# Kernel tuning notes

Measured on AMD Instinct MI355X. Metric: run time of the kernel, lower is better.

The kernel has to match this reference:

```python
import jax, jax.numpy as jnp
import numpy as np

N = 50000
E = 1600000
F_IN = 128
F_OUT = 64
NEG_SLOPE = 0.2


def setup_inputs() -> dict:
    key = jax.random.key(0)
    k1, k2, k3, k4, k5, k6 = jax.random.split(key, 6)
    x = jax.random.normal(k1, (N, F_IN), dtype=jnp.float32)
    edge_index = jax.random.randint(k2, (2, E), 0, N, dtype=jnp.int64)
    # GATConv params (heads=1): glorot-ish scale
    W = jax.random.normal(k3, (F_IN, F_OUT), dtype=jnp.float32) * (1.0 / np.sqrt(F_IN))
    att_src = jax.random.normal(k4, (F_OUT,), dtype=jnp.float32) * (1.0 / np.sqrt(F_OUT))
    att_dst = jax.random.normal(k5, (F_OUT,), dtype=jnp.float32) * (1.0 / np.sqrt(F_OUT))
    bias = jnp.zeros((F_OUT,), dtype=jnp.float32)
    return {"x": x, "edge_index": edge_index, "W": W, "att_src": att_src, "att_dst": att_dst, "bias": bias}


def _gat_forward(x, edge_index, W, att_src, att_dst, bias):
    n = x.shape[0]
    # add self loops (PyG GATConv default)
    loops = jnp.arange(n, dtype=edge_index.dtype)
    src = jnp.concatenate([edge_index[0], loops])  # [E+N]
    dst = jnp.concatenate([edge_index[1], loops])  # [E+N]

    h = x @ W                                      # [N, F_OUT]
    a_src = h @ att_src                            # [N]
    a_dst = h @ att_dst                            # [N]

    e = a_src[src] + a_dst[dst]                    # [E+N]
    e = jnp.where(e > 0, e, NEG_SLOPE * e)         # LeakyReLU(0.2)

    # softmax over edges grouped by destination node
    e_max = jax.ops.segment_max(e, dst, num_segments=n)     # [N]
    e_exp = jnp.exp(e - e_max[dst])                          # [E+N]
    e_sum = jax.ops.segment_sum(e_exp, dst, num_segments=n)  # [N]
    alpha = e_exp / e_sum[dst]                               # [E+N]

    msg = h[src] * alpha[:, None]                            # [E+N, F_OUT]
    out = jax.ops.segment_sum(msg, dst, num_segments=n)      # [N, F_OUT]
    out = out + bias
    return jax.nn.relu(out)


def reference(x, edge_index, W, att_src, att_dst, bias):
    return _gat_forward(x, edge_index, W, att_src, att_dst, bias)
```

## Files before the change

### kernel.cpp

```cpp
#include <hip/hip_runtime.h>

#define NN 50000
#define NE 1600000
#define FIN 128
#define FOUT 64
#define SLOPE 0.2f

#define NBC  63
#define NPC  800
#define CAPC 27500
#define NBF  1575
#define NPB  32
#define CAPB 1536
#define FBLK 522
#define CHC4 768
#define K2PB 8
#define FINB (NBC * K2PB)
#define GBLK 782
#define LW   136

typedef unsigned int u32;
typedef short short8 __attribute__((ext_vector_type(8)));
typedef float f32x4 __attribute__((ext_vector_type(4)));

__device__ __forceinline__ unsigned short f2bf(float f) {
    u32 u = __float_as_uint(f);
    u += 0x7FFFu + ((u >> 16) & 1u);
    return (unsigned short)(u >> 16);
}
__device__ __forceinline__ float bf2f(unsigned short s) {
    return __uint_as_float(((u32)s) << 16);
}

__global__ __launch_bounds__(256) void fill_k(
        const int* __restrict__ ei, int* __restrict__ ccur,
        u32* __restrict__ cstage) {
    __shared__ int cnt[4][64];
    __shared__ int gb[64];
    __shared__ int cur[64];
    const int tid = threadIdx.x, wv = tid >> 6;
    ((int*)cnt)[tid] = 0;
    __syncthreads();
    const int4* sd4 = (const int4*)(ei + NE);
    const int4* ss4 = (const int4*)ei;
    const int lo = blockIdx.x * CHC4, hi = min(NE / 4, lo + CHC4);
    for (int i = lo + tid; i < hi; i += 256) {
        int4 d = sd4[i];
        atomicAdd(&cnt[wv][d.x / NPC], 1);
        atomicAdd(&cnt[wv][d.y / NPC], 1);
        atomicAdd(&cnt[wv][d.z / NPC], 1);
        atomicAdd(&cnt[wv][d.w / NPC], 1);
    }
    __syncthreads();
    if (tid < NBC) {
        int tot = cnt[0][tid] + cnt[1][tid] + cnt[2][tid] + cnt[3][tid];
        gb[tid] = tot ? atomicAdd(&ccur[tid], tot) : 0;
        cur[tid] = 0;
    }
    __syncthreads();
    for (int i = lo + tid; i < hi; i += 256) {
        int4 d = sd4[i];
        int4 s = ss4[i];
        int b, pos;
        b = d.x / NPC; pos = gb[b] + atomicAdd(&cur[b], 1);
        if (pos < CAPC) cstage[b * CAPC + pos] = (u32)s.x | ((u32)(d.x - b * NPC) << 16);
        b = d.y / NPC; pos = gb[b] + atomicAdd(&cur[b], 1);
        if (pos < CAPC) cstage[b * CAPC + pos] = (u32)s.y | ((u32)(d.y - b * NPC) << 16);
        b = d.z / NPC; pos = gb[b] + atomicAdd(&cur[b], 1);
        if (pos < CAPC) cstage[b * CAPC + pos] = (u32)s.z | ((u32)(d.z - b * NPC) << 16);
        b = d.w / NPC; pos = gb[b] + atomicAdd(&cur[b], 1);
        if (pos < CAPC) cstage[b * CAPC + pos] = (u32)s.w | ((u32)(d.w - b * NPC) << 16);
    }
}

union FgLds {
    unsigned short Wt[64 * LW];
    struct { int cnt[4][32]; int gb[32]; int cur[32]; } f;
};

__global__ __launch_bounds__(256) void fg_k(
        const u32* __restrict__ cstage, const int* __restrict__ ccur,
        int* __restrict__ fcur, u32* __restrict__ fstage,
        const float* __restrict__ x, const float* __restrict__ W,
        const float* __restrict__ att_s, const float* __restrict__ att_d,
        unsigned short* __restrict__ h, float* __restrict__ a_src,
        float* __restrict__ a_dst) {
    __shared__ FgLds L;
    const int tid = threadIdx.x;

    if (blockIdx.x < FINB) {
        const int bin = blockIdx.x / K2PB, sub = blockIdx.x % K2PB;
        const int size = min(ccur[bin], CAPC);
        const int qs = (size + K2PB - 1) / K2PB;
        const int lo = sub * qs, hi = min(size, lo + qs);
        const u32* src = cstage + (size_t)bin * CAPC;
        const int wv = tid >> 6;
        ((int*)L.f.cnt)[tid & 127] = 0;
        __syncthreads();
        for (int i = lo + tid; i < hi; i += 256)
            atomicAdd(&L.f.cnt[wv][(src[i] >> 16) >> 5], 1);
        __syncthreads();
        if (tid < 25) {
            int tot = L.f.cnt[0][tid] + L.f.cnt[1][tid]
                    + L.f.cnt[2][tid] + L.f.cnt[3][tid];
            L.f.gb[tid] = tot ? atomicAdd(&fcur[bin * 25 + tid], tot) : 0;
            L.f.cur[tid] = 0;
        }
        __syncthreads();
        for (int i = lo + tid; i < hi; i += 256) {
            u32 w = src[i];
            int dl = w >> 16;
            int f = dl >> 5;
            int pos = L.f.gb[f] + atomicAdd(&L.f.cur[f], 1);
            if (pos < CAPB)
                fstage[(size_t)(bin * 25 + f) * CAPB + pos] =
                    (w & 0xFFFFu) | ((u32)(dl & 31) << 16);
        }
    } else {
        unsigned short* Wt = L.Wt;
        const int node0 = (blockIdx.x - FINB) * 64;
        for (int i = tid; i < 128 * 16; i += 256) {
            int k = i >> 4, f = (i & 15) * 4;
            float4 w4 = ((const float4*)W)[i];
            Wt[(f + 0) * LW + k] = f2bf(w4.x);
            Wt[(f + 1) * LW + k] = f2bf(w4.y);
            Wt[(f + 2) * LW + k] = f2bf(w4.z);
            Wt[(f + 3) * LW + k] = f2bf(w4.w);
        }
        const int wv = tid >> 6, lane = tid & 63;
        const int q = lane >> 4, mr = lane & 15;
        const int row = node0 + wv * 16 + mr;
        const bool valid = row < NN;
        const float4* x4 = (const float4*)x;

        short8 afr[4];
        #pragma unroll
        for (int ks = 0; ks < 4; ++ks) {
            float4 f0 = make_float4(0.f, 0.f, 0.f, 0.f), f1 = f0;
            if (valid) {
                f0 = x4[(size_t)row * 32 + ks * 8 + q * 2];
                f1 = x4[(size_t)row * 32 + ks * 8 + q * 2 + 1];
            }
            short8 a;
            a[0] = (short)f2bf(f0.x); a[1] = (short)f2bf(f0.y);
            a[2] = (short)f2bf(f0.z); a[3] = (short)f2bf(f0.w);
            a[4] = (short)f2bf(f1.x); a[5] = (short)f2bf(f1.y);
            a[6] = (short)f2bf(f1.z); a[7] = (short)f2bf(f1.w);
            afr[ks] = a;
        }
        __syncthreads();

        f32x4 acc[4] = {{0,0,0,0},{0,0,0,0},{0,0,0,0},{0,0,0,0}};
        #pragma unroll
        for (int ks = 0; ks < 4; ++ks) {
            #pragma unroll
            for (int nt = 0; nt < 4; ++nt) {
                short8 b = *(const short8*)(Wt + (nt * 16 + mr) * LW + ks * 32 + q * 8);
                acc[nt] = __builtin_amdgcn_mfma_f32_16x16x32_bf16(afr[ks], b, acc[nt], 0, 0, 0);
            }
        }
        float atts[4], attd[4];
        #pragma unroll
        for (int nt = 0; nt < 4; ++nt) {
            atts[nt] = att_s[nt * 16 + mr];
            attd[nt] = att_d[nt * 16 + mr];
        }
        #pragma unroll
        for (int r = 0; r < 4; ++r) {
            int node = node0 + wv * 16 + q * 4 + r;
            float ps = 0.f, pd = 0.f;
            #pragma unroll
            for (int nt = 0; nt < 4; ++nt) {
                float v = acc[nt][r];
                if (node < NN) h[(size_t)node * 64 + nt * 16 + mr] = f2bf(v);
                ps += v * atts[nt];
                pd += v * attd[nt];
            }
            #pragma unroll
            for (int off = 8; off > 0; off >>= 1) {
                ps += __shfl_xor(ps, off);
                pd += __shfl_xor(pd, off);
            }
            if (mr == 0 && node < NN) { a_src[node] = ps; a_dst[node] = pd; }
        }
    }
}

__global__ __launch_bounds__(256) void agg_k(
        const u32* __restrict__ staging, const int* __restrict__ bcur,
        const float* __restrict__ a_src, const float* __restrict__ a_dst,
        const ushort4* __restrict__ h4, const float* __restrict__ bias,
        float* __restrict__ out) {
    const int bkt = blockIdx.x;
    const int node0 = bkt << 5;
    if (node0 >= NN) return;
    const int nNodes = min(NPB, NN - node0);
    const int bsize = min(bcur[bkt], CAPB);
    const u32* stg = staging + (size_t)bkt * CAPB;
    const int tid = threadIdx.x, wv = tid >> 6, lane = tid & 63;

    __shared__ u32 pk[CAPB];
    __shared__ unsigned short ssrc[CAPB];
    __shared__ int lcnt[NPB];
    __shared__ int lbase[NPB + 1];
    __shared__ int lcur[NPB];
    float* evals = (float*)pk;

    for (int j = tid; j < bsize; j += 256) pk[j] = stg[j];
    if (tid < NPB) lcnt[tid] = 0;
    __syncthreads();
    for (int j = tid; j < bsize; j += 256)
        atomicAdd(&lcnt[pk[j] >> 16], 1);
    __syncthreads();
    if (tid < 64) {
        int v = (tid < NPB) ? lcnt[tid] : 0;
        #pragma unroll
        for (int off = 1; off < NPB; off <<= 1) {
            int u = __shfl_up(v, off);
            if (tid >= off) v += u;
        }
        if (tid < NPB) lbase[tid + 1] = v;
        if (tid == 0) lbase[0] = 0;
    }
    if (tid >= 64 && tid < 64 + NPB) lcur[tid - 64] = 0;
    __syncthreads();
    for (int j = tid; j < bsize; j += 256) {
        u32 w = pk[j];
        int ld = w >> 16;
        int pos = lbase[ld] + atomicAdd(&lcur[ld], 1);
        ssrc[pos] = (unsigned short)(w & 0xFFFFu);
    }
    __syncthreads();

    const int q = lane >> 4, ql = lane & 15;
    const float4 b4 = ((const float4*)bias)[ql];
    #pragma unroll
    for (int rnd = 0; rnd < 2; ++rnd) {
        const int ln = rnd * 16 + wv * 4 + q;
        if (ln >= nNodes) continue;
        const int n = node0 + ln;
        const int st = lbase[ln], deg = lbase[ln + 1] - st;
        const float ad = a_dst[n];
        float es = a_src[n] + ad; es = es > 0.f ? es : SLOPE * es;
        const float ps = __expf(es);
        float sum = 0.f;
        for (int j = ql; j < deg; j += 16) {
            int s = ssrc[st + j];
            float e = a_src[s] + ad; e = e > 0.f ? e : SLOPE * e;
            float pe = __expf(e);
            evals[st + j] = pe;
            sum += pe;
        }
        sum += __shfl_xor(sum, 8); sum += __shfl_xor(sum, 4);
        sum += __shfl_xor(sum, 2); sum += __shfl_xor(sum, 1);
        const float inv = 1.f / (sum + ps);

        ushort4 hs = h4[(size_t)n * 16 + ql];
        float a0 = ps * bf2f(hs.x), a1 = ps * bf2f(hs.y);
        float a2 = ps * bf2f(hs.z), a3 = ps * bf2f(hs.w);
        int j = 0;
        for (; j + 4 <= deg; j += 4) {
            int s0 = ssrc[st + j], s1 = ssrc[st + j + 1];
            int s2 = ssrc[st + j + 2], s3 = ssrc[st + j + 3];
            float e0 = evals[st + j], e1 = evals[st + j + 1];
            float e2 = evals[st + j + 2], e3 = evals[st + j + 3];
            ushort4 v0 = h4[(size_t)s0 * 16 + ql];
            ushort4 v1 = h4[(size_t)s1 * 16 + ql];
            ushort4 v2 = h4[(size_t)s2 * 16 + ql];
            ushort4 v3 = h4[(size_t)s3 * 16 + ql];
            a0 += e0 * bf2f(v0.x); a1 += e0 * bf2f(v0.y);
            a2 += e0 * bf2f(v0.z); a3 += e0 * bf2f(v0.w);
            a0 += e1 * bf2f(v1.x); a1 += e1 * bf2f(v1.y);
            a2 += e1 * bf2f(v1.z); a3 += e1 * bf2f(v1.w);
            a0 += e2 * bf2f(v2.x); a1 += e2 * bf2f(v2.y);
            a2 += e2 * bf2f(v2.z); a3 += e2 * bf2f(v2.w);
            a0 += e3 * bf2f(v3.x); a1 += e3 * bf2f(v3.y);
            a2 += e3 * bf2f(v3.z); a3 += e3 * bf2f(v3.w);
        }
        for (; j < deg; ++j) {
            int s = ssrc[st + j];
            float ev = evals[st + j];
            ushort4 hv = h4[(size_t)s * 16 + ql];
            a0 += ev * bf2f(hv.x); a1 += ev * bf2f(hv.y);
            a2 += ev * bf2f(hv.z); a3 += ev * bf2f(hv.w);
        }
        float4 o;
        o.x = a0 * inv + b4.x; o.x = o.x > 0.f ? o.x : 0.f;
        o.y = a1 * inv + b4.y; o.y = o.y > 0.f ? o.y : 0.f;
        o.z = a2 * inv + b4.z; o.z = o.z > 0.f ? o.z : 0.f;
        o.w = a3 * inv + b4.w; o.w = o.w > 0.f ? o.w : 0.f;
        ((float4*)out)[(size_t)n * 16 + ql] = o;
    }
}

extern "C" void kernel_launch(void* const* d_in, const int* in_sizes, int n_in,
                              void* d_out, int out_size, void* d_ws, size_t ws_size,
                              hipStream_t stream) {
    const float* x     = (const float*)d_in[0];
    const int*   ei    = (const int*)d_in[1];
    const float* W     = (const float*)d_in[2];
    const float* att_s = (const float*)d_in[3];
    const float* att_d = (const float*)d_in[4];
    const float* bias  = (const float*)d_in[5];
    float* out = (float*)d_out;

    unsigned short* h = (unsigned short*)d_ws;
    float* a_src  = (float*)(h + (size_t)NN * 64);
    float* a_dst  = a_src + NN;
    int*   ccur   = (int*)(a_dst + NN);
    int*   fcur   = ccur + 64;
    u32*   cstage = (u32*)(fcur + 1600);
    u32*   fstage = cstage + (size_t)NBC * CAPC;

    hipMemsetAsync(ccur, 0, (64 + 1600) * sizeof(int), stream);

    fill_k<<<FBLK, 256, 0, stream>>>(ei, ccur, cstage);
    fg_k<<<FINB + GBLK, 256, 0, stream>>>(cstage, ccur, fcur, fstage,
                                          x, W, att_s, att_d, h, a_src, a_dst);
    agg_k<<<NBF, 256, 0, stream>>>(fstage, fcur, a_src, a_dst,
                                   (const ushort4*)h, bias, out);
}
```

Baseline: 146.1 us.

## Use per-wave LDS cursors in binning, double fine-bin split, unroll gather by 8

The coarse and fine binning kernels now turn their per-wave LDS histograms into per-wave prefix offsets after the global atomic. Each wave then claims slots from its own counter instead of one shared block cursor, which cuts LDS atomic contention and drops the separate gb/cur arrays. The fine-binning pass splits each coarse bin across 16 blocks instead of 8 for more parallelism, at the cost of more global atomics on fcur. The aggregation loop unrolls the neighbor gather to 8 so more bf16 row loads are in flight, which raises register use.

```diff
diff --git a/kernel.cpp b/kernel.cpp
--- a/kernel.cpp
+++ b/kernel.cpp
@@ -14,7 +14,7 @@
 #define CAPB 1536
 #define FBLK 522
 #define CHC4 768
-#define K2PB 8
+#define K2PB 16
 #define FINB (NBC * K2PB)
 #define GBLK 782
 #define LW   136
@@ -36,8 +36,6 @@
         const int* __restrict__ ei, int* __restrict__ ccur,
         u32* __restrict__ cstage) {
     __shared__ int cnt[4][64];
-    __shared__ int gb[64];
-    __shared__ int cur[64];
     const int tid = threadIdx.x, wv = tid >> 6;
     ((int*)cnt)[tid] = 0;
     __syncthreads();
@@ -52,30 +50,35 @@
         atomicAdd(&cnt[wv][d.w / NPC], 1);
     }
     __syncthreads();
-    if (tid < NBC) {
-        int tot = cnt[0][tid] + cnt[1][tid] + cnt[2][tid] + cnt[3][tid];
-        gb[tid] = tot ? atomicAdd(&ccur[tid], tot) : 0;
-        cur[tid] = 0;
+    if (tid < 64) {
+        int c0 = cnt[0][tid], c1 = cnt[1][tid];
+        int c2 = cnt[2][tid], c3 = cnt[3][tid];
+        int tot = c0 + c1 + c2 + c3;
+        int base = tot ? atomicAdd(&ccur[tid], tot) : 0;
+        cnt[0][tid] = base;
+        cnt[1][tid] = base + c0;
+        cnt[2][tid] = base + c0 + c1;
+        cnt[3][tid] = base + c0 + c1 + c2;
     }
     __syncthreads();
     for (int i = lo + tid; i < hi; i += 256) {
         int4 d = sd4[i];
         int4 s = ss4[i];
         int b, pos;
-        b = d.x / NPC; pos = gb[b] + atomicAdd(&cur[b], 1);
+        b = d.x / NPC; pos = atomicAdd(&cnt[wv][b], 1);
         if (pos < CAPC) cstage[b * CAPC + pos] = (u32)s.x | ((u32)(d.x - b * NPC) << 16);
-        b = d.y / NPC; pos = gb[b] + atomicAdd(&cur[b], 1);
+        b = d.y / NPC; pos = atomicAdd(&cnt[wv][b], 1);
         if (pos < CAPC) cstage[b * CAPC + pos] = (u32)s.y | ((u32)(d.y - b * NPC) << 16);
-        b = d.z / NPC; pos = gb[b] + atomicAdd(&cur[b], 1);
+        b = d.z / NPC; pos = atomicAdd(&cnt[wv][b], 1);
         if (pos < CAPC) cstage[b * CAPC + pos] = (u32)s.z | ((u32)(d.z - b * NPC) << 16);
-        b = d.w / NPC; pos = gb[b] + atomicAdd(&cur[b], 1);
+        b = d.w / NPC; pos = atomicAdd(&cnt[wv][b], 1);
         if (pos < CAPC) cstage[b * CAPC + pos] = (u32)s.w | ((u32)(d.w - b * NPC) << 16);
     }
 }
 
 union FgLds {
     unsigned short Wt[64 * LW];
-    struct { int cnt[4][32]; int gb[32]; int cur[32]; } f;
+    int fcnt[4][32];
 };
 
 __global__ __launch_bounds__(256) void fg_k(
@@ -95,23 +98,27 @@
         const int lo = sub * qs, hi = min(size, lo + qs);
         const u32* src = cstage + (size_t)bin * CAPC;
         const int wv = tid >> 6;
-        ((int*)L.f.cnt)[tid & 127] = 0;
+        ((int*)L.fcnt)[tid & 127] = 0;
         __syncthreads();
         for (int i = lo + tid; i < hi; i += 256)
-            atomicAdd(&L.f.cnt[wv][(src[i] >> 16) >> 5], 1);
+            atomicAdd(&L.fcnt[wv][(src[i] >> 16) >> 5], 1);
         __syncthreads();
         if (tid < 25) {
-            int tot = L.f.cnt[0][tid] + L.f.cnt[1][tid]
-                    + L.f.cnt[2][tid] + L.f.cnt[3][tid];
-            L.f.gb[tid] = tot ? atomicAdd(&fcur[bin * 25 + tid], tot) : 0;
-            L.f.cur[tid] = 0;
+            int c0 = L.fcnt[0][tid], c1 = L.fcnt[1][tid];
+            int c2 = L.fcnt[2][tid], c3 = L.fcnt[3][tid];
+            int tot = c0 + c1 + c2 + c3;
+            int base = tot ? atomicAdd(&fcur[bin * 25 + tid], tot) : 0;
+            L.fcnt[0][tid] = base;
+            L.fcnt[1][tid] = base + c0;
+            L.fcnt[2][tid] = base + c0 + c1;
+            L.fcnt[3][tid] = base + c0 + c1 + c2;
         }
         __syncthreads();
         for (int i = lo + tid; i < hi; i += 256) {
             u32 w = src[i];
             int dl = w >> 16;
             int f = dl >> 5;
-            int pos = L.f.gb[f] + atomicAdd(&L.f.cur[f], 1);
+            int pos = atomicAdd(&L.fcnt[wv][f], 1);
             if (pos < CAPB)
                 fstage[(size_t)(bin * 25 + f) * CAPB + pos] =
                     (w & 0xFFFFu) | ((u32)(dl & 31) << 16);
@@ -259,23 +266,19 @@
         float a0 = ps * bf2f(hs.x), a1 = ps * bf2f(hs.y);
         float a2 = ps * bf2f(hs.z), a3 = ps * bf2f(hs.w);
         int j = 0;
-        for (; j + 4 <= deg; j += 4) {
-            int s0 = ssrc[st + j], s1 = ssrc[st + j + 1];
-            int s2 = ssrc[st + j + 2], s3 = ssrc[st + j + 3];
-            float e0 = evals[st + j], e1 = evals[st + j + 1];
-            float e2 = evals[st + j + 2], e3 = evals[st + j + 3];
-            ushort4 v0 = h4[(size_t)s0 * 16 + ql];
-            ushort4 v1 = h4[(size_t)s1 * 16 + ql];
-            ushort4 v2 = h4[(size_t)s2 * 16 + ql];
-            ushort4 v3 = h4[(size_t)s3 * 16 + ql];
-            a0 += e0 * bf2f(v0.x); a1 += e0 * bf2f(v0.y);
-            a2 += e0 * bf2f(v0.z); a3 += e0 * bf2f(v0.w);
-            a0 += e1 * bf2f(v1.x); a1 += e1 * bf2f(v1.y);
-            a2 += e1 * bf2f(v1.z); a3 += e1 * bf2f(v1.w);
-            a0 += e2 * bf2f(v2.x); a1 += e2 * bf2f(v2.y);
-            a2 += e2 * bf2f(v2.z); a3 += e2 * bf2f(v2.w);
-            a0 += e3 * bf2f(v3.x); a1 += e3 * bf2f(v3.y);
-            a2 += e3 * bf2f(v3.z); a3 += e3 * bf2f(v3.w);
+        for (; j + 8 <= deg; j += 8) {
+            ushort4 v[8];
+            float ev[8];
+            #pragma unroll
+            for (int t = 0; t < 8; ++t) {
+                v[t] = h4[(size_t)ssrc[st + j + t] * 16 + ql];
+                ev[t] = evals[st + j + t];
+            }
+            #pragma unroll
+            for (int t = 0; t < 8; ++t) {
+                a0 += ev[t] * bf2f(v[t].x); a1 += ev[t] * bf2f(v[t].y);
+                a2 += ev[t] * bf2f(v[t].z); a3 += ev[t] * bf2f(v[t].w);
+            }
         }
         for (; j < deg; ++j) {
             int s = ssrc[st + j];
```

Result: slower. 149.5 us (+2.3%).
